# Optimization experiments

Measured on AMD Instinct MI355X. Metric: run time of the kernel, lower is better.

Reference implementation:

```python
import jax, jax.numpy as jnp
import numpy as np

B, T, D = 1, 2048, 1024
H = 16
SEM_DIM, GEO_DIM, ATTN_DIM = 512, 512, 1024
ROPE_BASE = 10000.0
NEG = -1e9


def setup_inputs() -> dict:
    key = jax.random.key(0)
    ks = jax.random.split(key, 10)
    s = 0.02
    return {
        "x": jax.random.normal(ks[0], (B, T, D), jnp.float32),
        "wq_sem": jax.random.normal(ks[1], (D, SEM_DIM), jnp.float32) * s,
        "wk_sem": jax.random.normal(ks[2], (D, SEM_DIM), jnp.float32) * s,
        "wq_geo": jax.random.normal(ks[3], (D, GEO_DIM), jnp.float32) * s,
        "wk_geo": jax.random.normal(ks[4], (D, GEO_DIM), jnp.float32) * s,
        "wv": jax.random.normal(ks[5], (D, ATTN_DIM), jnp.float32) * s,
        "wo": jax.random.normal(ks[6], (ATTN_DIM, D), jnp.float32) * s,
        "k_sem_null": jax.random.normal(ks[7], (SEM_DIM,), jnp.float32) * s,
        "k_geo_null": jax.random.normal(ks[8], (GEO_DIM,), jnp.float32) * s,
        "v_null": jax.random.normal(ks[9], (ATTN_DIM,), jnp.float32) * s,
    }


def _heads(y, hd):
    b, t, _ = y.shape
    return y.reshape(b, t, H, hd).transpose(0, 2, 1, 3)  # [B,H,T,hd]


def _rope(x, cos, sin):
    # x: [B,H,T,hd], cos/sin: [T,hd//2] (rotate-half convention)
    hd = x.shape[-1]
    x1, x2 = x[..., : hd // 2], x[..., hd // 2 :]
    c = cos[None, None]
    sn = sin[None, None]
    return jnp.concatenate([x1 * c - x2 * sn, x2 * c + x1 * sn], axis=-1)


def _forward(x, wq_sem, wk_sem, wq_geo, wk_geo, wv, wo, k_sem_null, k_geo_null, v_null):
    b, t, _ = x.shape
    sem_hd = wq_sem.shape[1] // H
    geo_hd = wq_geo.shape[1] // H
    v_hd = wv.shape[1] // H
    sem_scale = 1.0 / np.sqrt(sem_hd)
    geo_scale = 1.0 / np.sqrt(geo_hd)

    qs = _heads(x @ wq_sem, sem_hd)
    ks = _heads(x @ wk_sem, sem_hd)
    qg = _heads(x @ wq_geo, geo_hd)
    kg = _heads(x @ wk_geo, geo_hd)
    v = _heads(x @ wv, v_hd)

    # RoPE on geometric branch only
    pos = jnp.arange(t, dtype=jnp.float32)
    inv_freq = 1.0 / (ROPE_BASE ** (jnp.arange(0, geo_hd, 2, dtype=jnp.float32) / geo_hd))
    ang = pos[:, None] * inv_freq[None, :]  # [T, geo_hd//2]
    cos, sin = jnp.cos(ang), jnp.sin(ang)
    qg = _rope(qg, cos, sin)
    kg = _rope(kg, cos, sin)

    # prepend null KV slot (not rotated, always attendable)
    ksn = jnp.broadcast_to(k_sem_null.reshape(1, 1, H, sem_hd).transpose(0, 2, 1, 3), (b, H, 1, sem_hd))
    kgn = jnp.broadcast_to(k_geo_null.reshape(1, 1, H, geo_hd).transpose(0, 2, 1, 3), (b, H, 1, geo_hd))
    vn = jnp.broadcast_to(v_null.reshape(1, 1, H, v_hd).transpose(0, 2, 1, 3), (b, H, 1, v_hd))
    ks_full = jnp.concatenate([ksn, ks], axis=2)  # [B,H,T+1,sem_hd]
    kg_full = jnp.concatenate([kgn, kg], axis=2)
    v_full = jnp.concatenate([vn, v], axis=2)

    # decoupled scores in fp32: sem*sem_scale + geo*geo_scale
    scores = (
        jnp.einsum("bhqd,bhkd->bhqk", qs, ks_full).astype(jnp.float32) * sem_scale
        + jnp.einsum("bhqd,bhkd->bhqk", qg, kg_full).astype(jnp.float32) * geo_scale
    )

    # causal mask over real tokens; null slot (key index 0) always visible
    causal = jnp.tril(jnp.ones((t, t), dtype=bool))
    mask = jnp.concatenate([jnp.ones((t, 1), dtype=bool), causal], axis=1)  # [T, T+1]
    scores = jnp.where(mask[None, None], scores, NEG)

    probs = jax.nn.softmax(scores, axis=-1).astype(v.dtype)
    out = jnp.einsum("bhqk,bhkd->bhqd", probs, v_full)  # [B,H,T,v_hd]
    out = out.transpose(0, 2, 1, 3).reshape(b, t, H * v_hd)
    return out @ wo


def reference(x, wq_sem, wk_sem, wq_geo, wk_geo, wv, wo, k_sem_null, k_geo_null, v_null):
    return _forward(x, wq_sem, wk_sem, wq_geo, wk_geo, wv, wo, k_sem_null, k_geo_null, v_null)
```

## Files before the change

### kernel.cpp

```cpp
#include <hip/hip_runtime.h>
#include <hip/hip_bf16.h>

typedef __hip_bfloat16 bf16;
typedef __attribute__((ext_vector_type(8))) short bf16x8;
typedef __attribute__((ext_vector_type(4))) short bf16x4;
typedef __attribute__((ext_vector_type(4))) float f32x4;

#define TSEQ   2048
#define DMODEL 1024
#define NHEAD  16
#define KST    2112
#define SCALE  0.17677669529663687f
#define LN1E4_16 0.5756462732485115f

__device__ __forceinline__ unsigned short f2bf(float f) {
    union { bf16 h; unsigned short u; } x;
    x.h = __float2bfloat16(f);
    return x.u;
}
__device__ __forceinline__ float bf2f(unsigned short u) {
    return __uint_as_float(((unsigned int)u) << 16);
}

__device__ __forceinline__ void gload_lds16(const void* g, void* l) {
    __builtin_amdgcn_global_load_lds(
        (const __attribute__((address_space(1))) void*)g,
        (__attribute__((address_space(3))) void*)l, 16, 0, 0);
}

__global__ __launch_bounds__(256) void prep_all(
    const float* __restrict__ X,
    const float* __restrict__ wqs, const float* __restrict__ wks,
    const float* __restrict__ wqg, const float* __restrict__ wkg,
    const float* __restrict__ wv,  const float* __restrict__ wo,
    const float* __restrict__ ksn, const float* __restrict__ kgn,
    const float* __restrict__ vn,
    unsigned short* __restrict__ Xb,
    unsigned short* __restrict__ WcatT, unsigned short* __restrict__ WoT,
    unsigned short* __restrict__ Kc, unsigned short* __restrict__ Vg)
{
    __shared__ float T[64][65];
    const int bx = blockIdx.x;
    const int tid = threadIdx.x;
    if (bx < 2048) {
        int i = (bx * 256 + tid) * 4;
        float4 v = *(const float4*)(X + i);
        ushort4 o;
        o.x = f2bf(v.x); o.y = f2bf(v.y); o.z = f2bf(v.z); o.w = f2bf(v.w);
        *(ushort4*)(Xb + i) = o;
    } else if (bx < 3584) {
        const int idx = bx - 2048;
        const int z = idx >> 8, rem = idx & 255;
        const int cx = rem & 15, ry = rem >> 4;
        const float* src; unsigned short* dst; int C;
        switch (z) {
            case 0: src = wqs; dst = WcatT;               C = 512;  break;
            case 1: src = wks; dst = WcatT + 512  * 1024; C = 512;  break;
            case 2: src = wqg; dst = WcatT + 1024 * 1024; C = 512;  break;
            case 3: src = wkg; dst = WcatT + 1536 * 1024; C = 512;  break;
            case 4: src = wv;  dst = WcatT + 2048 * 1024; C = 1024; break;
            default: src = wo; dst = WoT;                 C = 1024; break;
        }
        const int c0 = cx * 64;
        if (c0 >= C) return;
        const int r0 = ry * 64;
        #pragma unroll
        for (int i = 0; i < 16; ++i) {
            int id2 = tid + 256 * i;
            int r = id2 >> 6, c = id2 & 63;
            T[r][c] = src[(size_t)(r0 + r) * C + c0 + c];
        }
        __syncthreads();
        #pragma unroll
        for (int i = 0; i < 16; ++i) {
            int id2 = tid + 256 * i;
            int cc = id2 >> 6, rr = id2 & 63;
            dst[(size_t)(c0 + cc) * 1024 + r0 + rr] = f2bf(T[rr][cc]);
        }
    } else {
        const int h = bx - 3584;
        const int d = tid & 63, g = tid >> 6;
        if (g == 0)
            Kc[((size_t)h * KST + 0) * 64 + d] =
                f2bf(d < 32 ? ksn[h * 32 + d] : kgn[h * 32 + d - 32]);
        if (g == 1)
            Vg[((size_t)h * 64 + d) * KST + 0] = f2bf(vn[h * 64 + d]);
        for (int fk = 2049 + g; fk < KST; fk += 4) {
            Kc[((size_t)h * KST + fk) * 64 + d] = 0;
            Vg[((size_t)h * 64 + d) * KST + fk] = 0;
        }
    }
}

__global__ __launch_bounds__(256) void gemm_proj_fused(
    const unsigned short* __restrict__ A,
    const unsigned short* __restrict__ Bt,
    unsigned short* __restrict__ Qc,
    unsigned short* __restrict__ Kc,
    unsigned short* __restrict__ Vg)
{
    __shared__ __align__(16) unsigned short Abuf[64 * 32];
    __shared__ __align__(16) unsigned short Bbuf[128 * 32];
    const int n0 = blockIdx.x * 128, m0 = blockIdx.y * 64;
    const int tid = threadIdx.x, l = tid & 63, wv = tid >> 6;
    const int wr = wv >> 1, wc = wv & 1;
    const int lr = l & 15, lg = l >> 4, kf = lg * 8;

    const int arow = wv * 16 + (l >> 2);
    const int aseg = (l & 3) * 8;

    f32x4 acc[2][4];
    #pragma unroll
    for (int i = 0; i < 2; ++i)
        #pragma unroll
        for (int j = 0; j < 4; ++j) acc[i][j] = (f32x4){0.f, 0.f, 0.f, 0.f};

    for (int k0 = 0; k0 < 1024; k0 += 32) {
        gload_lds16(A + (size_t)(m0 + arow) * 1024 + k0 + aseg, &Abuf[wv * 512]);
        #pragma unroll
        for (int it = 0; it < 2; ++it) {
            int brow = it * 64 + wv * 16 + (l >> 2);
            gload_lds16(Bt + (size_t)(n0 + brow) * 1024 + k0 + aseg,
                        &Bbuf[(it * 256 + wv * 64) * 8]);
        }
        __syncthreads();
        bf16x8 af[2], bfv[4];
        #pragma unroll
        for (int mf = 0; mf < 2; ++mf)
            af[mf] = *(const bf16x8*)&Abuf[(wr * 32 + mf * 16 + lr) * 32 + kf];
        #pragma unroll
        for (int nf = 0; nf < 4; ++nf)
            bfv[nf] = *(const bf16x8*)&Bbuf[(wc * 64 + nf * 16 + lr) * 32 + kf];
        #pragma unroll
        for (int mf = 0; mf < 2; ++mf)
            #pragma unroll
            for (int nf = 0; nf < 4; ++nf)
                acc[mf][nf] = __builtin_amdgcn_mfma_f32_16x16x32_bf16(
                    af[mf], bfv[nf], acc[mf][nf], 0, 0, 0);
        __syncthreads();
    }

    const int sec = n0 >> 9;
    if (sec <= 1) {
        unsigned short* dst = (sec == 0) ? Qc : Kc;
        const int tstr  = (sec == 0) ? TSEQ : KST;
        const int fkoff = (sec == 0) ? 0 : 1;
        const float sc  = (sec == 0) ? SCALE : 1.0f;
        #pragma unroll
        for (int mf = 0; mf < 2; ++mf)
            #pragma unroll
            for (int nf = 0; nf < 4; ++nf) {
                int col = (n0 & 511) + wc * 64 + nf * 16 + lr;
                int h = col >> 5, d = col & 31;
                #pragma unroll
                for (int reg = 0; reg < 4; ++reg) {
                    int q = m0 + wr * 32 + mf * 16 + lg * 4 + reg;
                    dst[((size_t)h * tstr + q + fkoff) * 64 + d] =
                        f2bf(acc[mf][nf][reg] * sc);
                }
            }
    } else if (sec <= 3) {
        unsigned short* dst = (sec == 2) ? Qc : Kc;
        const int tstr  = (sec == 2) ? TSEQ : KST;
        const int fkoff = (sec == 2) ? 0 : 1;
        const float sc  = (sec == 2) ? SCALE : 1.0f;
        const float invf = __expf(-(float)lr * LN1E4_16);
        #pragma unroll
        for (int mf = 0; mf < 2; ++mf)
            #pragma unroll
            for (int reg = 0; reg < 4; ++reg) {
                int q = m0 + wr * 32 + mf * 16 + lg * 4 + reg;
                float s, c;
                __sincosf((float)q * invf, &s, &c);
                #pragma unroll
                for (int nfp = 0; nfp < 2; ++nfp) {
                    int nf0 = nfp * 2;
                    int colbase = (n0 & 511) + wc * 64 + nf0 * 16;
                    int h = colbase >> 5;
                    float x1 = acc[mf][nf0][reg], x2 = acc[mf][nf0 + 1][reg];
                    size_t base = ((size_t)h * tstr + q + fkoff) * 64 + 32;
                    dst[base + lr]      = f2bf((x1 * c - x2 * s) * sc);
                    dst[base + lr + 16] = f2bf((x2 * c + x1 * s) * sc);
                }
            }
    } else {
        #pragma unroll
        for (int nf = 0; nf < 4; ++nf) {
            int colr = (n0 - 2048) + wc * 64 + nf * 16 + lr;
            int h = colr >> 6, dv = colr & 63;
            size_t rowbase = ((size_t)h * 64 + dv) * KST;
            #pragma unroll
            for (int mf = 0; mf < 2; ++mf)
                #pragma unroll
                for (int reg = 0; reg < 4; ++reg) {
                    int q = m0 + wr * 32 + mf * 16 + lg * 4 + reg;
                    Vg[rowbase + q + 1] = f2bf(acc[mf][nf][reg]);
                }
        }
    }
}

__global__ __launch_bounds__(256) void gemm_out(const unsigned short* __restrict__ A,
                                                const unsigned short* __restrict__ Bt,
                                                float* __restrict__ C)
{
    __shared__ __align__(16) unsigned short Abuf[64 * 32];
    __shared__ __align__(16) unsigned short Bbuf[64 * 32];
    const int n0 = blockIdx.x * 64, m0 = blockIdx.y * 64;
    const int tid = threadIdx.x, l = tid & 63, wv = tid >> 6;
    const int wr = wv >> 1, wc = wv & 1;
    const int lr = l & 15, lg = l >> 4, kf = lg * 8;

    const int arow = wv * 16 + (l >> 2);
    const int aseg = (l & 3) * 8;

    f32x4 acc[2][2];
    #pragma unroll
    for (int i = 0; i < 2; ++i)
        #pragma unroll
        for (int j = 0; j < 2; ++j) acc[i][j] = (f32x4){0.f, 0.f, 0.f, 0.f};

    for (int k0 = 0; k0 < 1024; k0 += 32) {
        gload_lds16(A  + (size_t)(m0 + arow) * 1024 + k0 + aseg, &Abuf[wv * 512]);
        gload_lds16(Bt + (size_t)(n0 + arow) * 1024 + k0 + aseg, &Bbuf[wv * 512]);
        __syncthreads();
        bf16x8 af[2], bfv[2];
        #pragma unroll
        for (int mf = 0; mf < 2; ++mf)
            af[mf] = *(const bf16x8*)&Abuf[(wr * 32 + mf * 16 + lr) * 32 + kf];
        #pragma unroll
        for (int nf = 0; nf < 2; ++nf)
            bfv[nf] = *(const bf16x8*)&Bbuf[(wc * 32 + nf * 16 + lr) * 32 + kf];
        #pragma unroll
        for (int mf = 0; mf < 2; ++mf)
            #pragma unroll
            for (int nf = 0; nf < 2; ++nf)
                acc[mf][nf] = __builtin_amdgcn_mfma_f32_16x16x32_bf16(
                    af[mf], bfv[nf], acc[mf][nf], 0, 0, 0);
        __syncthreads();
    }
    #pragma unroll
    for (int mf = 0; mf < 2; ++mf)
        #pragma unroll
        for (int nf = 0; nf < 2; ++nf)
            #pragma unroll
            for (int reg = 0; reg < 4; ++reg) {
                int row = m0 + wr * 32 + mf * 16 + lg * 4 + reg;
                int col = n0 + wc * 32 + nf * 16 + lr;
                C[(size_t)row * DMODEL + col] = acc[mf][nf][reg];
            }
}

__global__ __launch_bounds__(256) void attn_mfma(
    const unsigned short* __restrict__ Qc,
    const unsigned short* __restrict__ Kc,
    const unsigned short* __restrict__ Vg,
    unsigned short* __restrict__ attnO,
    unsigned short* __restrict__ OpA,
    unsigned short* __restrict__ OpB,
    float2* __restrict__ ml)
{
    __shared__ __align__(16) unsigned short KsL[2][64 * 64];
    __shared__ __align__(16) unsigned short VsL[2][64 * 64];
    __shared__ __align__(16) unsigned short Ps[128 * 64];

    const int ib = blockIdx.x;
    const int hp = ib & 7;
    const int j  = ib >> 3;
    const int h  = hp * 2 + (j & 1);
    const int item = j >> 1;

    int qb, part, np;
    {
        int i = item;
        if (i < 16)      { np = 4; qb = 15 - (i >> 2); part = i & 3; }
        else if (i < 28) { int jj = i - 16; np = 3; qb = 11 - jj / 3; part = jj % 3; }
        else if (i < 38) { int jj = i - 28; np = 2; qb = 7 - (jj >> 1); part = jj & 1; }
        else             { np = 1; qb = 2 - (i - 38); part = 0; }
    }
    const int nt = 2 * qb + 3;
    const int bsz = nt / np, rem = nt % np;
    const int t0 = part * bsz + (part < rem ? part : rem);
    const int t1 = t0 + bsz + (part < rem ? 1 : 0);

    const int q0 = qb * 128;
    const int tid = threadIdx.x, l = tid & 63, w = tid >> 6;
    const int lr = l & 15, lg = l >> 4;

    bf16x8 qa[2][2];
    #pragma unroll
    for (int rg = 0; rg < 2; ++rg) {
        int qr = q0 + w * 32 + rg * 16 + lr;
        qa[rg][0] = *(const bf16x8*)&Qc[((size_t)h * TSEQ + qr) * 64 + lg * 8];
        qa[rg][1] = *(const bf16x8*)&Qc[((size_t)h * TSEQ + qr) * 64 + 32 + lg * 8];
    }

    const int sc8 = (((l & 7) ^ ((l >> 3) & 7))) * 8;
    const int r0s = (w * 2 + 0) * 8 + (l >> 3);
    const int r1s = (w * 2 + 1) * 8 + (l >> 3);
    const unsigned short* Kh = Kc + (((size_t)h * KST) << 6);
    const unsigned short* Vh = Vg + (size_t)h * 64 * KST;

#define STAGE_KV(bufi, fk0_) do {                                              \
        gload_lds16(Kh + (((size_t)((fk0_) + r0s)) << 6) + sc8,                \
                    &KsL[bufi][(w * 2 + 0) * 512]);                            \
        gload_lds16(Kh + (((size_t)((fk0_) + r1s)) << 6) + sc8,                \
                    &KsL[bufi][(w * 2 + 1) * 512]);                            \
        gload_lds16(Vh + (size_t)r0s * KST + (fk0_) + sc8,                     \
                    &VsL[bufi][(w * 2 + 0) * 512]);                            \
        gload_lds16(Vh + (size_t)r1s * KST + (fk0_) + sc8,                     \
                    &VsL[bufi][(w * 2 + 1) * 512]);                            \
    } while (0)

    f32x4 o[2][4];
    #pragma unroll
    for (int rg = 0; rg < 2; ++rg)
        #pragma unroll
        for (int i = 0; i < 4; ++i) o[rg][i] = (f32x4){0.f, 0.f, 0.f, 0.f};
    float m[2]  = {-1e30f, -1e30f};
    float ll[2] = {0.f, 0.f};

    int buf = 0;
    STAGE_KV(0, t0 * 64);
    asm volatile("s_waitcnt vmcnt(0)" ::: "memory");
    __builtin_amdgcn_s_barrier();

    for (int kb = t0; kb < t1; ++kb) {
        const int fk0 = kb * 64;
        if (kb + 1 < t1) STAGE_KV(buf ^ 1, fk0 + 64);

        const unsigned short* Ksb = &KsL[buf][0];
        const unsigned short* Vsb = &VsL[buf][0];

        f32x4 sa[2][4];
        #pragma unroll
        for (int rg = 0; rg < 2; ++rg)
            #pragma unroll
            for (int i = 0; i < 4; ++i) sa[rg][i] = (f32x4){0.f, 0.f, 0.f, 0.f};
        __builtin_amdgcn_s_setprio(1);
        #pragma unroll
        for (int ks = 0; ks < 2; ++ks) {
            int dd = lg * 8 + ks * 32;
            #pragma unroll
            for (int nf = 0; nf < 4; ++nf) {
                int kkc = nf * 16 + lr;
                bf16x8 kbf = *(const bf16x8*)&Ksb[kkc * 64 + (dd ^ ((kkc & 7) << 3))];
                sa[0][nf] = __builtin_amdgcn_mfma_f32_16x16x32_bf16(kbf, qa[0][ks], sa[0][nf], 0, 0, 0);
                sa[1][nf] = __builtin_amdgcn_mfma_f32_16x16x32_bf16(kbf, qa[1][ks], sa[1][nf], 0, 0, 0);
            }
        }
        __builtin_amdgcn_s_setprio(0);

        const bool needmask = (fk0 + 62 > q0 + w * 32);
        #pragma unroll
        for (int rg = 0; rg < 2; ++rg) {
            const int q = q0 + w * 32 + rg * 16 + lr;
            float mt = -1e30f;
            if (needmask) {
                #pragma unroll
                for (int nf = 0; nf < 4; ++nf)
                    #pragma unroll
                    for (int reg = 0; reg < 4; ++reg) {
                        int fk = fk0 + nf * 16 + lg * 4 + reg;
                        float val = (fk <= q + 1) ? sa[rg][nf][reg] : -1e9f;
                        sa[rg][nf][reg] = val;
                        mt = fmaxf(mt, val);
                    }
            } else {
                #pragma unroll
                for (int nf = 0; nf < 4; ++nf)
                    #pragma unroll
                    for (int reg = 0; reg < 4; ++reg)
                        mt = fmaxf(mt, sa[rg][nf][reg]);
            }
            mt = fmaxf(mt, __shfl_xor(mt, 16, 64));
            mt = fmaxf(mt, __shfl_xor(mt, 32, 64));
            if (__any(mt > m[rg] + 8.0f)) {
                float mn = fmaxf(m[rg], mt);
                float alpha = __expf(m[rg] - mn);
                m[rg] = mn;
                ll[rg] *= alpha;
                #pragma unroll
                for (int nf = 0; nf < 4; ++nf)
                    #pragma unroll
                    for (int reg = 0; reg < 4; ++reg)
                        o[rg][nf][reg] *= alpha;
            }
            float rs = 0.0f;
            #pragma unroll
            for (int nf = 0; nf < 4; ++nf)
                #pragma unroll
                for (int reg = 0; reg < 4; ++reg) {
                    float p = __expf(sa[rg][nf][reg] - m[rg]);
                    sa[rg][nf][reg] = p;
                    rs += p;
                }
            rs += __shfl_xor(rs, 16, 64);
            rs += __shfl_xor(rs, 32, 64);
            ll[rg] += rs;

            int r = w * 32 + rg * 16 + lr;
            #pragma unroll
            for (int nf = 0; nf < 4; ++nf) {
                bf16x4 pk;
                pk[0] = f2bf(sa[rg][nf][0]); pk[1] = f2bf(sa[rg][nf][1]);
                pk[2] = f2bf(sa[rg][nf][2]); pk[3] = f2bf(sa[rg][nf][3]);
                int kk0 = nf * 16 + lg * 4;
                *(bf16x4*)&Ps[r * 64 + (kk0 ^ ((r & 7) << 3))] = pk;
            }
        }

        __builtin_amdgcn_s_setprio(1);
        #pragma unroll
        for (int ks = 0; ks < 2; ++ks) {
            int kk0 = lg * 8 + ks * 32;
            int swz = kk0 ^ ((lr & 7) << 3);
            bf16x8 pa0 = *(const bf16x8*)&Ps[(w * 32 + lr) * 64 + swz];
            bf16x8 pa1 = *(const bf16x8*)&Ps[(w * 32 + 16 + lr) * 64 + swz];
            #pragma unroll
            for (int nf = 0; nf < 4; ++nf) {
                int dv = nf * 16 + lr;
                bf16x8 vb = *(const bf16x8*)&Vsb[dv * 64 + (kk0 ^ ((dv & 7) << 3))];
                o[0][nf] = __builtin_amdgcn_mfma_f32_16x16x32_bf16(vb, pa0, o[0][nf], 0, 0, 0);
                o[1][nf] = __builtin_amdgcn_mfma_f32_16x16x32_bf16(vb, pa1, o[1][nf], 0, 0, 0);
            }
        }
        __builtin_amdgcn_s_setprio(0);

        asm volatile("s_waitcnt vmcnt(0)" ::: "memory");
        __builtin_amdgcn_s_barrier();
        buf ^= 1;
    }
#undef STAGE_KV

    const int sidx = h * 38 + item;
    unsigned short* Od = (np == 1) ? 0
        : ((sidx < 384) ? OpA + (size_t)sidx * 8192
                        : OpB + (size_t)(sidx - 384) * 8192);
    #pragma unroll
    for (int rg = 0; rg < 2; ++rg) {
        const float inv = 1.0f / ll[rg];
        const int q = q0 + w * 32 + rg * 16 + lr;
        if (np == 1) {
            #pragma unroll
            for (int nf = 0; nf < 4; ++nf) {
                ushort4 ov;
                ov.x = f2bf(o[rg][nf][0] * inv); ov.y = f2bf(o[rg][nf][1] * inv);
                ov.z = f2bf(o[rg][nf][2] * inv); ov.w = f2bf(o[rg][nf][3] * inv);
                *(ushort4*)&attnO[(size_t)q * DMODEL + h * 64 + nf * 16 + lg * 4] = ov;
            }
        } else {
            const int r = w * 32 + rg * 16 + lr;
            #pragma unroll
            for (int nf = 0; nf < 4; ++nf) {
                ushort4 ov;
                ov.x = f2bf(o[rg][nf][0] * inv); ov.y = f2bf(o[rg][nf][1] * inv);
                ov.z = f2bf(o[rg][nf][2] * inv); ov.w = f2bf(o[rg][nf][3] * inv);
                *(ushort4*)&Od[r * 64 + nf * 16 + lg * 4] = ov;
            }
            if (lg == 0)
                ml[sidx * 128 + r] = make_float2(m[rg], ll[rg]);
        }
    }
}

__global__ __launch_bounds__(256) void combine_wave(
    const unsigned short* __restrict__ OpA,
    const unsigned short* __restrict__ OpB,
    const float2* __restrict__ ml,
    unsigned short* __restrict__ attnO)
{
    const int qb = 3 + blockIdx.x;
    const int h  = blockIdx.y;
    int np, i0;
    if (qb >= 12)     { np = 4; i0 = (15 - qb) * 4; }
    else if (qb >= 8) { np = 3; i0 = 16 + (11 - qb) * 3; }
    else              { np = 2; i0 = 28 + (7 - qb) * 2; }
    const int sidx0 = h * 38 + i0;

    const int t = threadIdx.x;
    const int r = t & 127, dv0 = (t >> 7) * 32;

    float wt[4];
    float mm = -1e30f;
    #pragma unroll
    for (int p = 0; p < 4; ++p)
        if (p < np) mm = fmaxf(mm, ml[(sidx0 + p) * 128 + r].x);
    float tot = 0.0f;
    #pragma unroll
    for (int p = 0; p < 4; ++p) {
        wt[p] = 0.0f;
        if (p < np) {
            float2 v = ml[(sidx0 + p) * 128 + r];
            wt[p] = v.y * __expf(v.x - mm);
            tot += wt[p];
        }
    }
    const float inv = 1.0f / tot;

    float accv[32];
    #pragma unroll
    for (int c = 0; c < 32; ++c) accv[c] = 0.0f;
    #pragma unroll
    for (int p = 0; p < 4; ++p) {
        if (p < np) {
            int s = sidx0 + p;
            const unsigned short* Od = (s < 384)
                ? OpA + (size_t)s * 8192
                : OpB + (size_t)(s - 384) * 8192;
            #pragma unroll
            for (int c4 = 0; c4 < 8; ++c4) {
                ushort4 v = *(const ushort4*)&Od[r * 64 + dv0 + c4 * 4];
                accv[c4 * 4 + 0] += wt[p] * bf2f(v.x);
                accv[c4 * 4 + 1] += wt[p] * bf2f(v.y);
                accv[c4 * 4 + 2] += wt[p] * bf2f(v.z);
                accv[c4 * 4 + 3] += wt[p] * bf2f(v.w);
            }
        }
    }
    const int q = qb * 128 + r;
    #pragma unroll
    for (int c4 = 0; c4 < 8; ++c4) {
        ushort4 ov;
        ov.x = f2bf(accv[c4 * 4 + 0] * inv);
        ov.y = f2bf(accv[c4 * 4 + 1] * inv);
        ov.z = f2bf(accv[c4 * 4 + 2] * inv);
        ov.w = f2bf(accv[c4 * 4 + 3] * inv);
        *(ushort4*)&attnO[(size_t)q * DMODEL + h * 64 + dv0 + c4 * 4] = ov;
    }
}

extern "C" void kernel_launch(void* const* d_in, const int* in_sizes, int n_in,
                              void* d_out, int out_size, void* d_ws, size_t ws_size,
                              hipStream_t stream)
{
    const float* x      = (const float*)d_in[0];
    const float* wq_sem = (const float*)d_in[1];
    const float* wk_sem = (const float*)d_in[2];
    const float* wq_geo = (const float*)d_in[3];
    const float* wk_geo = (const float*)d_in[4];
    const float* wv     = (const float*)d_in[5];
    const float* wo     = (const float*)d_in[6];
    const float* ksn    = (const float*)d_in[7];
    const float* kgn    = (const float*)d_in[8];
    const float* vn     = (const float*)d_in[9];
    float* out = (float*)d_out;

    char* ws = (char*)d_ws;
    unsigned short* Xb    = (unsigned short*)(ws);
    unsigned short* attnO = (unsigned short*)(ws);
    unsigned short* WcatT = (unsigned short*)(ws + 4194304);
    unsigned short* OpA   = (unsigned short*)(ws + 4194304);
    unsigned short* WoT   = (unsigned short*)(ws + 10485760);
    unsigned short* Qc    = (unsigned short*)(ws + 12582912);
    unsigned short* Kc    = (unsigned short*)(ws + 16777216);
    unsigned short* Vg    = (unsigned short*)(ws + 21102592);
    unsigned short* OpB   = (unsigned short*)(ws + 25427968);
    float2*         ml    = (float2*)(ws + 29097984);

    prep_all<<<3600, 256, 0, stream>>>(x, wq_sem, wk_sem, wq_geo, wk_geo, wv, wo,
                                       ksn, kgn, vn, Xb, WcatT, WoT, Kc, Vg);

    gemm_proj_fused<<<dim3(24, 32), 256, 0, stream>>>(Xb, WcatT, Qc, Kc, Vg);

    attn_mfma<<<656, 256, 0, stream>>>(Qc, Kc, Vg, attnO, OpA, OpB, ml);
    combine_wave<<<dim3(13, NHEAD), 256, 0, stream>>>(OpA, OpB, ml, attnO);

    gemm_out<<<dim3(16, 32), 256, 0, stream>>>(attnO, WoT, out);
}
```

Before: 96.89 us.

## Deepen GEMM K-tile to 64 with XOR-swizzled LDS and widen output GEMM tile

Both projection GEMMs now stage 64-wide K slices per iteration instead of 32, which halves the number of barrier pairs per tile. The LDS layout uses an XOR swizzle on 16-byte segments to avoid bank conflicts on the fragment reads. The output GEMM tile grows from 64x64 to 64x128, so each block reuses its A tile across more columns, at the cost of fewer blocks (256) and more LDS and registers per block.

```diff
diff --git a/kernel.cpp b/kernel.cpp
--- a/kernel.cpp
+++ b/kernel.cpp
@@ -99,15 +99,12 @@
     unsigned short* __restrict__ Kc,
     unsigned short* __restrict__ Vg)
 {
-    __shared__ __align__(16) unsigned short Abuf[64 * 32];
-    __shared__ __align__(16) unsigned short Bbuf[128 * 32];
+    __shared__ __align__(16) unsigned short Abuf[64 * 64];
+    __shared__ __align__(16) unsigned short Bbuf[128 * 64];
     const int n0 = blockIdx.x * 128, m0 = blockIdx.y * 64;
     const int tid = threadIdx.x, l = tid & 63, wv = tid >> 6;
     const int wr = wv >> 1, wc = wv & 1;
-    const int lr = l & 15, lg = l >> 4, kf = lg * 8;
-
-    const int arow = wv * 16 + (l >> 2);
-    const int aseg = (l & 3) * 8;
+    const int lr = l & 15, lg = l >> 4;
 
     f32x4 acc[2][4];
     #pragma unroll
@@ -115,28 +112,44 @@
         #pragma unroll
         for (int j = 0; j < 4; ++j) acc[i][j] = (f32x4){0.f, 0.f, 0.f, 0.f};
 
-    for (int k0 = 0; k0 < 1024; k0 += 32) {
-        gload_lds16(A + (size_t)(m0 + arow) * 1024 + k0 + aseg, &Abuf[wv * 512]);
-        #pragma unroll
-        for (int it = 0; it < 2; ++it) {
-            int brow = it * 64 + wv * 16 + (l >> 2);
-            gload_lds16(Bt + (size_t)(n0 + brow) * 1024 + k0 + aseg,
-                        &Bbuf[(it * 256 + wv * 64) * 8]);
+    for (int k0 = 0; k0 < 1024; k0 += 64) {
+        #pragma unroll
+        for (int i = 0; i < 2; ++i) {
+            int c = wv * 128 + i * 64 + l;
+            int row = c >> 3, sseg = (c & 7) ^ (row & 7);
+            gload_lds16(A + (size_t)(m0 + row) * 1024 + k0 + sseg * 8,
+                        &Abuf[(wv * 128 + i * 64) * 8]);
+        }
+        #pragma unroll
+        for (int i = 0; i < 4; ++i) {
+            int c = wv * 256 + i * 64 + l;
+            int row = c >> 3, sseg = (c & 7) ^ (row & 7);
+            gload_lds16(Bt + (size_t)(n0 + row) * 1024 + k0 + sseg * 8,
+                        &Bbuf[(wv * 256 + i * 64) * 8]);
         }
         __syncthreads();
-        bf16x8 af[2], bfv[4];
-        #pragma unroll
-        for (int mf = 0; mf < 2; ++mf)
-            af[mf] = *(const bf16x8*)&Abuf[(wr * 32 + mf * 16 + lr) * 32 + kf];
-        #pragma unroll
-        for (int nf = 0; nf < 4; ++nf)
-            bfv[nf] = *(const bf16x8*)&Bbuf[(wc * 64 + nf * 16 + lr) * 32 + kf];
-        #pragma unroll
-        for (int mf = 0; mf < 2; ++mf)
-            #pragma unroll
-            for (int nf = 0; nf < 4; ++nf)
-                acc[mf][nf] = __builtin_amdgcn_mfma_f32_16x16x32_bf16(
-                    af[mf], bfv[nf], acc[mf][nf], 0, 0, 0);
+        #pragma unroll
+        for (int ks = 0; ks < 2; ++ks) {
+            bf16x8 af[2], bfv[4];
+            #pragma unroll
+            for (int mf = 0; mf < 2; ++mf) {
+                int rr = wr * 32 + mf * 16 + lr;
+                int seg = (ks * 4 + lg) ^ (rr & 7);
+                af[mf] = *(const bf16x8*)&Abuf[rr * 64 + seg * 8];
+            }
+            #pragma unroll
+            for (int nf = 0; nf < 4; ++nf) {
+                int rr = wc * 64 + nf * 16 + lr;
+                int seg = (ks * 4 + lg) ^ (rr & 7);
+                bfv[nf] = *(const bf16x8*)&Bbuf[rr * 64 + seg * 8];
+            }
+            #pragma unroll
+            for (int mf = 0; mf < 2; ++mf)
+                #pragma unroll
+                for (int nf = 0; nf < 4; ++nf)
+                    acc[mf][nf] = __builtin_amdgcn_mfma_f32_16x16x32_bf16(
+                        af[mf], bfv[nf], acc[mf][nf], 0, 0, 0);
+        }
         __syncthreads();
     }
 
@@ -204,49 +217,67 @@
                                                 const unsigned short* __restrict__ Bt,
                                                 float* __restrict__ C)
 {
-    __shared__ __align__(16) unsigned short Abuf[64 * 32];
-    __shared__ __align__(16) unsigned short Bbuf[64 * 32];
-    const int n0 = blockIdx.x * 64, m0 = blockIdx.y * 64;
+    __shared__ __align__(16) unsigned short Abuf[64 * 64];
+    __shared__ __align__(16) unsigned short Bbuf[128 * 64];
+    const int n0 = blockIdx.x * 128, m0 = blockIdx.y * 64;
     const int tid = threadIdx.x, l = tid & 63, wv = tid >> 6;
     const int wr = wv >> 1, wc = wv & 1;
-    const int lr = l & 15, lg = l >> 4, kf = lg * 8;
-
-    const int arow = wv * 16 + (l >> 2);
-    const int aseg = (l & 3) * 8;
-
-    f32x4 acc[2][2];
+    const int lr = l & 15, lg = l >> 4;
+
+    f32x4 acc[2][4];
     #pragma unroll
     for (int i = 0; i < 2; ++i)
         #pragma unroll
-        for (int j = 0; j < 2; ++j) acc[i][j] = (f32x4){0.f, 0.f, 0.f, 0.f};
-
-    for (int k0 = 0; k0 < 1024; k0 += 32) {
-        gload_lds16(A  + (size_t)(m0 + arow) * 1024 + k0 + aseg, &Abuf[wv * 512]);
-        gload_lds16(Bt + (size_t)(n0 + arow) * 1024 + k0 + aseg, &Bbuf[wv * 512]);
+        for (int j = 0; j < 4; ++j) acc[i][j] = (f32x4){0.f, 0.f, 0.f, 0.f};
+
+    for (int k0 = 0; k0 < 1024; k0 += 64) {
+        #pragma unroll
+        for (int i = 0; i < 2; ++i) {
+            int c = wv * 128 + i * 64 + l;
+            int row = c >> 3, sseg = (c & 7) ^ (row & 7);
+            gload_lds16(A + (size_t)(m0 + row) * 1024 + k0 + sseg * 8,
+                        &Abuf[(wv * 128 + i * 64) * 8]);
+        }
+        #pragma unroll
+        for (int i = 0; i < 4; ++i) {
+            int c = wv * 256 + i * 64 + l;
+            int row = c >> 3, sseg = (c & 7) ^ (row & 7);
+            gload_lds16(Bt + (size_t)(n0 + row) * 1024 + k0 + sseg * 8,
+                        &Bbuf[(wv * 256 + i * 64) * 8]);
+        }
         __syncthreads();
-        bf16x8 af[2], bfv[2];
-        #pragma unroll
-        for (int mf = 0; mf < 2; ++mf)
-            af[mf] = *(const bf16x8*)&Abuf[(wr * 32 + mf * 16 + lr) * 32 + kf];
-        #pragma unroll
-        for (int nf = 0; nf < 2; ++nf)
-            bfv[nf] = *(const bf16x8*)&Bbuf[(wc * 32 + nf * 16 + lr) * 32 + kf];
-        #pragma unroll
-        for (int mf = 0; mf < 2; ++mf)
-            #pragma unroll
-            for (int nf = 0; nf < 2; ++nf)
-                acc[mf][nf] = __builtin_amdgcn_mfma_f32_16x16x32_bf16(
-                    af[mf], bfv[nf], acc[mf][nf], 0, 0, 0);
+        #pragma unroll
+        for (int ks = 0; ks < 2; ++ks) {
+            bf16x8 af[2], bfv[4];
+            #pragma unroll
+            for (int mf = 0; mf < 2; ++mf) {
+                int rr = wr * 32 + mf * 16 + lr;
+                int seg = (ks * 4 + lg) ^ (rr & 7);
+                af[mf] = *(const bf16x8*)&Abuf[rr * 64 + seg * 8];
+            }
+            #pragma unroll
+            for (int nf = 0; nf < 4; ++nf) {
+                int rr = wc * 64 + nf * 16 + lr;
+                int seg = (ks * 4 + lg) ^ (rr & 7);
+                bfv[nf] = *(const bf16x8*)&Bbuf[rr * 64 + seg * 8];
+            }
+            #pragma unroll
+            for (int mf = 0; mf < 2; ++mf)
+                #pragma unroll
+                for (int nf = 0; nf < 4; ++nf)
+                    acc[mf][nf] = __builtin_amdgcn_mfma_f32_16x16x32_bf16(
+                        af[mf], bfv[nf], acc[mf][nf], 0, 0, 0);
+        }
         __syncthreads();
     }
     #pragma unroll
     for (int mf = 0; mf < 2; ++mf)
         #pragma unroll
-        for (int nf = 0; nf < 2; ++nf)
+        for (int nf = 0; nf < 4; ++nf)
             #pragma unroll
             for (int reg = 0; reg < 4; ++reg) {
                 int row = m0 + wr * 32 + mf * 16 + lg * 4 + reg;
-                int col = n0 + wc * 32 + nf * 16 + lr;
+                int col = n0 + wc * 64 + nf * 16 + lr;
                 C[(size_t)row * DMODEL + col] = acc[mf][nf][reg];
             }
 }
@@ -566,5 +597,5 @@
     attn_mfma<<<656, 256, 0, stream>>>(Qc, Kc, Vg, attnO, OpA, OpB, ml);
     combine_wave<<<dim3(13, NHEAD), 256, 0, stream>>>(OpA, OpB, ml, attnO);
 
-    gemm_out<<<dim3(16, 32), 256, 0, stream>>>(attnO, WoT, out);
-}
+    gemm_out<<<dim3(8, 32), 256, 0, stream>>>(attnO, WoT, out);
+}
```

New measurement: 91.09 us. 6.0% less time.
